# Optimization experiments

Measured on AMD Instinct MI355X. Metric: run time of the kernel, lower is better.

The kernel has to match this reference:

```python
import jax, jax.numpy as jnp
import numpy as np

N_NODES = 20000
N_EDGES = 320000
EMB = 128


def setup_inputs() -> dict:
    key = jax.random.key(0)
    ks = jax.random.split(key, 8)
    h = jax.random.normal(ks[0], (N_NODES, EMB), dtype=jnp.float32)
    W1 = jax.random.normal(ks[1], (2 * EMB, 4 * EMB), dtype=jnp.float32) / np.sqrt(2 * EMB)
    b1 = jnp.zeros((4 * EMB,), dtype=jnp.float32)
    W2 = jax.random.normal(ks[2], (4 * EMB, 1), dtype=jnp.float32) / np.sqrt(4 * EMB)
    b2 = jnp.zeros((1,), dtype=jnp.float32)
    # logistic-noise uniforms for RelaxedBernoulli rsample, kept away from {0,1}
    u = jax.random.uniform(ks[3], (N_EDGES,), dtype=jnp.float32, minval=1e-6, maxval=1.0 - 1e-6)
    row = jax.random.randint(ks[4], (N_EDGES,), 0, N_NODES, dtype=jnp.int32)
    col = jax.random.randint(ks[5], (N_EDGES,), 0, N_NODES, dtype=jnp.int32)
    edge_mask = -jnp.ones((N_EDGES,), dtype=jnp.int32)  # torch code initializes mask to -1
    return {"h": h, "W1": W1, "b1": b1, "W2": W2, "b2": b2,
            "u": u, "row": row, "col": col, "edge_mask": edge_mask, "hierarchy": 0}


def _segment_softmax(scores, seg, num_segments):
    m = jax.ops.segment_max(scores, seg, num_segments=num_segments)
    e = jnp.exp(scores - m[seg])
    s = jax.ops.segment_sum(e, seg, num_segments=num_segments)
    return e / s[seg]


TEMPERATURE = 1.0
RATIO = 0.5  # threshold for hard bernoulli


def reference(h, W1, b1, W2, b2, u, row, col, edge_mask, hierarchy):
    # edge gather + concat: [E, 2*EMB]
    edge_rep = jnp.concatenate([h[row], h[col]], axis=-1)
    # 2-layer MLP edge scorer -> [E]
    hid = jax.nn.relu(edge_rep @ W1 + b1)
    scores = (hid @ W2 + b2).reshape(-1)
    # segment softmax over edges grouped by source node (torch: softmax(edge_score, edge_index[0]))
    probs = _segment_softmax(scores, row, N_NODES)
    # RelaxedBernoulli(temperature, probs).rsample(): sigmoid((logits + logistic)/T)
    logits = jnp.log(probs) - jnp.log1p(-probs)
    logistic = jnp.log(u) - jnp.log1p(-u)
    y = jax.nn.sigmoid((logits + logistic) / TEMPERATURE)
    y_hard = (y > RATIO).astype(y.dtype)
    y_st = jax.lax.stop_gradient(y_hard - y) + y  # straight-through
    # edge_mask[y == 1] = hierarchy + 1
    new_mask = jnp.where(y_st == 1.0, jnp.int32(hierarchy + 1), edge_mask)
    c_idx = new_mask > 0
    s_idx = new_mask == -1
    causal_w = jnp.where(c_idx, scores, 0.0)
    spu_w = jnp.where(s_idx, -scores, 0.0)
    return scores, y_st, new_mask, causal_w, spu_w
```

## Files before the change

### kernel.cpp

```cpp
#include <hip/hip_runtime.h>
#include <math.h>

#define N_NODES 20000
#define N_EDGES 320000
#define EMB 128
#define HID 512
#define ROWS_PER_BLOCK 16
#define SC_CAP 2048
#define NCHUNK ((N_NODES + 1023) / 1024)

typedef float v2f __attribute__((ext_vector_type(2)));

#if defined(__has_builtin)
#if __has_builtin(__builtin_elementwise_fma)
#define V2FMA(a, b, c) __builtin_elementwise_fma((a), (b), (c))
#else
#define V2FMA(a, b, c) ((a) * (b) + (c))
#endif
#else
#define V2FMA(a, b, c) ((a) * (b) + (c))
#endif

__global__ void init_deg(int* __restrict__ deg, int* __restrict__ offs) {
    int i = blockIdx.x * 256 + threadIdx.x;
    if (i < N_NODES) deg[i] = 0;
    if (i == 0) offs[N_NODES] = N_EDGES;
}

#define TM 128
#define TN 128
#define BK 8
#define NTILES (EMB / BK)
#define GEMM_MT ((N_NODES + TM - 1) / TM)
#define GEMM_BLOCKS (8 * GEMM_MT)
#define HIST_BLOCKS ((N_EDGES + 255) / 256)

__global__ __launch_bounds__(256) void gemm_hist(
    const float* __restrict__ h, const float* __restrict__ W1,
    const float* __restrict__ b1, float* __restrict__ P, float* __restrict__ Q,
    const int* __restrict__ row, int* __restrict__ deg)
{
    const int bid = blockIdx.x;
    const int tid = threadIdx.x;

    if (bid >= GEMM_BLOCKS) {
        const int e = (bid - GEMM_BLOCKS) * 256 + tid;
        if (e < N_EDGES) atomicAdd(&deg[row[e]], 1);
        return;
    }

    __shared__ float As[2][BK][TM + 4];
    __shared__ float Bs[2][BK][TN];

    const int nt = bid & 7;
    const int mt = bid >> 3;
    const int m_base = mt * TM;

    const int a_m = tid >> 1;
    const int a_k = (tid & 1) << 2;
    const int  row_a = m_base + a_m;
    const bool a_ok  = row_a < N_NODES;
    const float* __restrict__ hrow = h + (size_t)row_a * EMB + a_k;

    const int b_k = tid >> 5;
    const int b_n = (tid & 31) << 2;
    const int w_row_off = (nt < 4) ? 0 : 128;
    const int w_col     = (nt & 3) * TN + b_n;
    const float* __restrict__ wrow = W1 + (size_t)(w_row_off + b_k) * HID + w_col;

    const int ty = tid >> 4, tx = tid & 15;
    const int cm = ty << 2, cn = tx << 2;

    v2f acc[8][4] = {};

    float4 pa, pb;
    pa = make_float4(0.f, 0.f, 0.f, 0.f);
    if (a_ok) pa = *(const float4*)(hrow);
    pb = *(const float4*)(wrow);
    As[0][a_k + 0][a_m] = pa.x;
    As[0][a_k + 1][a_m] = pa.y;
    As[0][a_k + 2][a_m] = pa.z;
    As[0][a_k + 3][a_m] = pa.w;
    *(float4*)&Bs[0][b_k][b_n] = pb;
    __syncthreads();

    for (int t = 0; t < NTILES; ++t) {
        const int cur = t & 1;
        if (t + 1 < NTILES) {
            const int k0 = (t + 1) * BK;
            pa = make_float4(0.f, 0.f, 0.f, 0.f);
            if (a_ok) pa = *(const float4*)(hrow + k0);
            pb = *(const float4*)(wrow + (size_t)k0 * HID);
        }

#pragma unroll
        for (int kk = 0; kk < BK; ++kk) {
            float a[8];
            *(float4*)&a[0] = *(const float4*)&As[cur][kk][cm];
            *(float4*)&a[4] = *(const float4*)&As[cur][kk][cm + 64];
            float4 b0 = *(const float4*)&Bs[cur][kk][cn];
            float4 b1v = *(const float4*)&Bs[cur][kk][cn + 64];
            v2f bp[4] = {(v2f){b0.x, b0.y}, (v2f){b0.z, b0.w},
                         (v2f){b1v.x, b1v.y}, (v2f){b1v.z, b1v.w}};
#pragma unroll
            for (int i = 0; i < 8; ++i) {
                v2f ai = (v2f){a[i], a[i]};
#pragma unroll
                for (int j = 0; j < 4; ++j)
                    acc[i][j] = V2FMA(ai, bp[j], acc[i][j]);
            }
        }

        if (t + 1 < NTILES) {
            const int nxt = 1 - cur;
            As[nxt][a_k + 0][a_m] = pa.x;
            As[nxt][a_k + 1][a_m] = pa.y;
            As[nxt][a_k + 2][a_m] = pa.z;
            As[nxt][a_k + 3][a_m] = pa.w;
            *(float4*)&Bs[nxt][b_k][b_n] = pb;
            __syncthreads();
        }
    }

    const bool  isP = (nt < 4);
    const int   col_base = (nt & 3) * TN;
    float* __restrict__ dstbase = isP ? P : Q;

    v2f bias[4] = {{0.f,0.f},{0.f,0.f},{0.f,0.f},{0.f,0.f}};
    if (isP) {
        float4 bv0 = *(const float4*)(b1 + col_base + cn);
        float4 bv1 = *(const float4*)(b1 + col_base + cn + 64);
        bias[0] = (v2f){bv0.x, bv0.y};
        bias[1] = (v2f){bv0.z, bv0.w};
        bias[2] = (v2f){bv1.x, bv1.y};
        bias[3] = (v2f){bv1.z, bv1.w};
    }

#pragma unroll
    for (int i = 0; i < 8; ++i) {
        const int r = m_base + cm + (i < 4 ? i : 64 + i - 4);
        if (r < N_NODES) {
            float* dst = dstbase + (size_t)r * HID + col_base;
            v2f c0 = acc[i][0] + bias[0], c1 = acc[i][1] + bias[1];
            v2f c2 = acc[i][2] + bias[2], c3 = acc[i][3] + bias[3];
            *(float4*)(dst + cn)      = make_float4(c0.x, c0.y, c1.x, c1.y);
            *(float4*)(dst + cn + 64) = make_float4(c2.x, c2.y, c3.x, c3.y);
        }
    }
}

__device__ __forceinline__ int wave_incl_scan(int v, int lane) {
#pragma unroll
    for (int off = 1; off < 64; off <<= 1) {
        int t = __shfl_up(v, off, 64);
        if (lane >= off) v += t;
    }
    return v;
}

__global__ __launch_bounds__(1024) void scan_part(const int* __restrict__ deg,
                                                  int* __restrict__ part,
                                                  int* __restrict__ totals) {
    __shared__ int wsum[16];
    const int tid = threadIdx.x, lane = tid & 63, w = tid >> 6;
    const int i = blockIdx.x * 1024 + tid;
    int v = (i < N_NODES) ? deg[i] : 0;
    int incl = wave_incl_scan(v, lane);
    if (lane == 63) wsum[w] = incl;
    __syncthreads();
    if (w == 0) {
        int x = (lane < 16) ? wsum[lane] : 0;
        int xs = wave_incl_scan(x, lane);
        if (lane < 16) wsum[lane] = xs - x;
        if (lane == 15) totals[blockIdx.x] = xs;
    }
    __syncthreads();
    if (i < N_NODES) part[i] = wsum[w] + incl - v;
}

__global__ __launch_bounds__(1024) void scan_apply(const int* __restrict__ part,
                                                   const int* __restrict__ totals,
                                                   int* __restrict__ cursor,
                                                   int* __restrict__ offs) {
    __shared__ int carry_s;
    const int tid = threadIdx.x;
    if (tid < 64) {
        int v = (tid < NCHUNK) ? totals[tid] : 0;
        int incl = wave_incl_scan(v, tid);
        if (tid == (int)blockIdx.x) carry_s = incl - v;
    }
    __syncthreads();
    const int i = blockIdx.x * 1024 + tid;
    if (i < N_NODES) {
        int o = part[i] + carry_s;
        cursor[i] = o;
        offs[i] = o;
    }
}

__global__ void scatter_edges(const int* __restrict__ row, const int* __restrict__ col,
                              int* __restrict__ cursor, int2* __restrict__ rc2) {
    int e = blockIdx.x * 256 + threadIdx.x;
    if (e >= N_EDGES) return;
    int r = row[e];
    int pos = atomicAdd(&cursor[r], 1);
    rc2[pos] = make_int2(e, (r << 16) | col[e]);
}

__global__ __launch_bounds__(256) void fused_edge(
    const float* __restrict__ P, const float* __restrict__ Q,
    const float* __restrict__ W2, const float* __restrict__ b2,
    const int2* __restrict__ rc2, const int* __restrict__ offs,
    const float* __restrict__ u, const int* __restrict__ edge_mask,
    const int* __restrict__ hierarchy,
    float* __restrict__ scores, float* __restrict__ out_y,
    float* __restrict__ out_mask, float* __restrict__ out_causal,
    float* __restrict__ out_spu)
{
    __shared__ float sc_lds[SC_CAP];

    const int r0 = blockIdx.x * ROWS_PER_BLOCK;
    const int r1 = (r0 + ROWS_PER_BLOCK < N_NODES) ? r0 + ROWS_PER_BLOCK : N_NODES;
    const int e0 = offs[r0];
    const int e1 = offs[r1];
    const int tid = threadIdx.x, lane = tid & 63, w = tid >> 6;
    const int j0 = lane << 2;

    const float4 w0 = *(const float4*)(W2 + j0);
    const float4 w1 = *(const float4*)(W2 + 256 + j0);
    const float bias2 = b2[0];

    for (int i0 = e0 + (w << 1); i0 < e1; i0 += 8) {
        const int  iA   = i0;
        const bool hasB = (i0 + 1) < e1;
        const int  iB   = hasB ? i0 + 1 : i0;

        const int2 eA = rc2[iA];
        const int2 eB = rc2[iB];
        const int rA = ((unsigned)eA.y) >> 16, cA = eA.y & 0xFFFF;
        const int rB = ((unsigned)eB.y) >> 16, cB = eB.y & 0xFFFF;
        const float* __restrict__ pA = P + (size_t)rA * HID;
        const float* __restrict__ qA = Q + (size_t)cA * HID;
        const float* __restrict__ pB = P + (size_t)rB * HID;
        const float* __restrict__ qB = Q + (size_t)cB * HID;

        float4 pA0 = *(const float4*)(pA + j0);
        float4 pA1 = *(const float4*)(pA + 256 + j0);
        float4 qA0 = *(const float4*)(qA + j0);
        float4 qA1 = *(const float4*)(qA + 256 + j0);
        float4 pB0 = *(const float4*)(pB + j0);
        float4 pB1 = *(const float4*)(pB + 256 + j0);
        float4 qB0 = *(const float4*)(qB + j0);
        float4 qB1 = *(const float4*)(qB + 256 + j0);

        float sA = 0.0f, sB = 0.0f;
        sA = fmaf(fmaxf(pA0.x + qA0.x, 0.0f), w0.x, sA);
        sA = fmaf(fmaxf(pA0.y + qA0.y, 0.0f), w0.y, sA);
        sA = fmaf(fmaxf(pA0.z + qA0.z, 0.0f), w0.z, sA);
        sA = fmaf(fmaxf(pA0.w + qA0.w, 0.0f), w0.w, sA);
        sA = fmaf(fmaxf(pA1.x + qA1.x, 0.0f), w1.x, sA);
        sA = fmaf(fmaxf(pA1.y + qA1.y, 0.0f), w1.y, sA);
        sA = fmaf(fmaxf(pA1.z + qA1.z, 0.0f), w1.z, sA);
        sA = fmaf(fmaxf(pA1.w + qA1.w, 0.0f), w1.w, sA);
        sB = fmaf(fmaxf(pB0.x + qB0.x, 0.0f), w0.x, sB);
        sB = fmaf(fmaxf(pB0.y + qB0.y, 0.0f), w0.y, sB);
        sB = fmaf(fmaxf(pB0.z + qB0.z, 0.0f), w0.z, sB);
        sB = fmaf(fmaxf(pB0.w + qB0.w, 0.0f), w0.w, sB);
        sB = fmaf(fmaxf(pB1.x + qB1.x, 0.0f), w1.x, sB);
        sB = fmaf(fmaxf(pB1.y + qB1.y, 0.0f), w1.y, sB);
        sB = fmaf(fmaxf(pB1.z + qB1.z, 0.0f), w1.z, sB);
        sB = fmaf(fmaxf(pB1.w + qB1.w, 0.0f), w1.w, sB);

#pragma unroll
        for (int off = 32; off > 0; off >>= 1) {
            sA += __shfl_down(sA, off, 64);
            sB += __shfl_down(sB, off, 64);
        }

        if (lane == 0) {
            float scA = sA + bias2;
            scores[eA.x] = scA;
            int liA = iA - e0;
            if (liA < SC_CAP) sc_lds[liA] = scA;
            if (hasB) {
                float scB = sB + bias2;
                scores[eB.x] = scB;
                int liB = iB - e0;
                if (liB < SC_CAP) sc_lds[liB] = scB;
            }
        }
    }
    __syncthreads();

    const int hv = hierarchy[0];
    for (int r = r0 + w; r < r1; r += 4) {
        const int es = offs[r], ee = offs[r + 1];
        const int d = ee - es;
        if (d == 0) continue;

        float m = -INFINITY;
        for (int j = lane; j < d; j += 64) {
            int li = es - e0 + j;
            float s = (li < SC_CAP) ? sc_lds[li] : scores[rc2[es + j].x];
            m = fmaxf(m, s);
        }
#pragma unroll
        for (int off = 32; off > 0; off >>= 1)
            m = fmaxf(m, __shfl_down(m, off, 64));
        m = __shfl(m, 0, 64);

        float ssum = 0.0f;
        for (int j = lane; j < d; j += 64) {
            int li = es - e0 + j;
            float s = (li < SC_CAP) ? sc_lds[li] : scores[rc2[es + j].x];
            ssum += expf(s - m);
        }
#pragma unroll
        for (int off = 32; off > 0; off >>= 1)
            ssum += __shfl_down(ssum, off, 64);
        ssum = __shfl(ssum, 0, 64);

        for (int j = lane; j < d; j += 64) {
            int li = es - e0 + j;
            float s = (li < SC_CAP) ? sc_lds[li] : scores[rc2[es + j].x];
            float p = expf(s - m) / ssum;
            float logits = logf(p) - log1pf(-p);
            int oe = rc2[es + j].x;
            float uu = u[oe];
            float L = logf(uu) - log1pf(-uu);
            float y = 1.0f / (1.0f + expf(-(logits + L)));
            bool hard = y > 0.5f;
            int mm = hard ? (hv + 1) : edge_mask[oe];
            out_y[oe]      = hard ? 1.0f : 0.0f;
            out_mask[oe]   = (float)mm;
            out_causal[oe] = (mm > 0)   ?  s : 0.0f;
            out_spu[oe]    = (mm == -1) ? -s : 0.0f;
        }
    }
}

extern "C" void kernel_launch(void* const* d_in, const int* in_sizes, int n_in,
                              void* d_out, int out_size, void* d_ws, size_t ws_size,
                              hipStream_t stream) {
    const float* h_ptr = (const float*)d_in[0];
    const float* W1    = (const float*)d_in[1];
    const float* b1    = (const float*)d_in[2];
    const float* W2    = (const float*)d_in[3];
    const float* b2    = (const float*)d_in[4];
    const float* u     = (const float*)d_in[5];
    const int*   row   = (const int*)d_in[6];
    const int*   col   = (const int*)d_in[7];
    const int*   emask = (const int*)d_in[8];
    const int*   hier  = (const int*)d_in[9];

    float* out        = (float*)d_out;
    float* scores     = out;
    float* out_y      = out + (size_t)N_EDGES;
    float* out_mask   = out + 2 * (size_t)N_EDGES;
    float* out_causal = out + 3 * (size_t)N_EDGES;
    float* out_spu    = out + 4 * (size_t)N_EDGES;

    float* P      = (float*)d_ws;
    float* Qm     = P + (size_t)N_NODES * HID;
    int2*  rc2    = (int2*)(Qm + (size_t)N_NODES * HID);
    int*   deg    = (int*)(rc2 + N_EDGES);
    int*   cursor = deg + N_NODES;
    int*   offs   = cursor + N_NODES;
    int*   part   = offs + N_NODES + 1;
    int*   totals = part + N_NODES;

    hipLaunchKernelGGL(init_deg, dim3((N_NODES + 255) / 256), dim3(256), 0, stream,
                       deg, offs);

    hipLaunchKernelGGL(gemm_hist, dim3(GEMM_BLOCKS + HIST_BLOCKS), dim3(256), 0, stream,
                       h_ptr, W1, b1, P, Qm, row, deg);

    hipLaunchKernelGGL(scan_part, dim3(NCHUNK), dim3(1024), 0, stream, deg, part, totals);
    hipLaunchKernelGGL(scan_apply, dim3(NCHUNK), dim3(1024), 0, stream,
                       part, totals, cursor, offs);
    hipLaunchKernelGGL(scatter_edges, dim3((N_EDGES + 255) / 256), dim3(256), 0, stream,
                       row, col, cursor, rc2);

    hipLaunchKernelGGL(fused_edge, dim3((N_NODES + ROWS_PER_BLOCK - 1) / ROWS_PER_BLOCK),
                       dim3(256), 0, stream,
                       P, Qm, W2, b2, rc2, offs, u, emask, hier,
                       scores, out_y, out_mask, out_causal, out_spu);
}
```

Baseline: 287.4 us.

## Process edges per source row with reused P row and coalesced unpermute pass

```diff
diff --git a/kernel.cpp b/kernel.cpp
--- a/kernel.cpp
+++ b/kernel.cpp
@@ -199,144 +199,165 @@
 }
 
 __global__ void scatter_edges(const int* __restrict__ row, const int* __restrict__ col,
-                              int* __restrict__ cursor, int2* __restrict__ rc2) {
+                              int* __restrict__ cursor,
+                              unsigned short* __restrict__ cols16,
+                              int* __restrict__ inv) {
     int e = blockIdx.x * 256 + threadIdx.x;
     if (e >= N_EDGES) return;
     int r = row[e];
     int pos = atomicAdd(&cursor[r], 1);
-    rc2[pos] = make_int2(e, (r << 16) | col[e]);
+    cols16[pos] = (unsigned short)col[e];
+    inv[e] = pos;
 }
 
 __global__ __launch_bounds__(256) void fused_edge(
     const float* __restrict__ P, const float* __restrict__ Q,
     const float* __restrict__ W2, const float* __restrict__ b2,
-    const int2* __restrict__ rc2, const int* __restrict__ offs,
+    const unsigned short* __restrict__ cols16, const int* __restrict__ offs,
+    float2* __restrict__ tmp)
+{
+    __shared__ float sc_lds[SC_CAP];
+
+    const int r0 = blockIdx.x * ROWS_PER_BLOCK;
+    const int r1 = (r0 + ROWS_PER_BLOCK < N_NODES) ? r0 + ROWS_PER_BLOCK : N_NODES;
+    const int e0 = offs[r0];
+    const int tid = threadIdx.x, lane = tid & 63, w = tid >> 6;
+    const int j0 = lane << 2;
+
+    const float4 w0 = *(const float4*)(W2 + j0);
+    const float4 w1 = *(const float4*)(W2 + 256 + j0);
+    const float bias2 = b2[0];
+
+    for (int r = r0 + w; r < r1; r += 4) {
+        const int es = offs[r], ee = offs[r + 1];
+        const int d = ee - es;
+        if (d == 0) continue;
+
+        const float* __restrict__ prow = P + (size_t)r * HID;
+        const float4 p0 = *(const float4*)(prow + j0);
+        const float4 p1 = *(const float4*)(prow + 256 + j0);
+
+        for (int base = 0; base < d; base += 64) {
+            const int nch = (d - base < 64) ? d - base : 64;
+            int mycol = 0;
+            if (lane < nch) mycol = (int)cols16[es + base + lane];
+
+#define QL(k, bb, d0, d1) { \
+                int c_ = __shfl(mycol, (bb) + (k), 64); \
+                const float* __restrict__ q_ = Q + (size_t)c_ * HID; \
+                d0 = *(const float4*)(q_ + j0); \
+                d1 = *(const float4*)(q_ + 256 + j0); }
+
+            float4 q00,q01,q10,q11,q20,q21,q30,q31;
+            QL(0,0,q00,q01); QL(1,0,q10,q11); QL(2,0,q20,q21); QL(3,0,q30,q31);
+
+            for (int b = 0; b < nch; b += 4) {
+                float4 n00,n01,n10,n11,n20,n21,n30,n31;
+                const bool more = (b + 4) < nch;
+                if (more) {
+                    QL(0,b+4,n00,n01); QL(1,b+4,n10,n11);
+                    QL(2,b+4,n20,n21); QL(3,b+4,n30,n31);
+                }
+
+                float s0, s1, s2, s3;
+#define DOT8(qa, qb, sd) { \
+                    float t_ = 0.0f; \
+                    t_ = fmaf(fmaxf(p0.x + qa.x, 0.0f), w0.x, t_); \
+                    t_ = fmaf(fmaxf(p0.y + qa.y, 0.0f), w0.y, t_); \
+                    t_ = fmaf(fmaxf(p0.z + qa.z, 0.0f), w0.z, t_); \
+                    t_ = fmaf(fmaxf(p0.w + qa.w, 0.0f), w0.w, t_); \
+                    t_ = fmaf(fmaxf(p1.x + qb.x, 0.0f), w1.x, t_); \
+                    t_ = fmaf(fmaxf(p1.y + qb.y, 0.0f), w1.y, t_); \
+                    t_ = fmaf(fmaxf(p1.z + qb.z, 0.0f), w1.z, t_); \
+                    t_ = fmaf(fmaxf(p1.w + qb.w, 0.0f), w1.w, t_); \
+                    sd = t_; }
+                DOT8(q00,q01,s0); DOT8(q10,q11,s1);
+                DOT8(q20,q21,s2); DOT8(q30,q31,s3);
+
+#pragma unroll
+                for (int off = 32; off > 0; off >>= 1) {
+                    s0 += __shfl_down(s0, off, 64);
+                    s1 += __shfl_down(s1, off, 64);
+                    s2 += __shfl_down(s2, off, 64);
+                    s3 += __shfl_down(s3, off, 64);
+                }
+
+                if (lane == 0) {
+                    const int nv = nch - b;
+                    const int libase = es - e0 + base + b;
+                    { float sc = s0 + bias2; int li = libase;
+                      if (li < SC_CAP) sc_lds[li] = sc; else tmp[e0 + li].x = sc; }
+                    if (nv > 1) { float sc = s1 + bias2; int li = libase + 1;
+                      if (li < SC_CAP) sc_lds[li] = sc; else tmp[e0 + li].x = sc; }
+                    if (nv > 2) { float sc = s2 + bias2; int li = libase + 2;
+                      if (li < SC_CAP) sc_lds[li] = sc; else tmp[e0 + li].x = sc; }
+                    if (nv > 3) { float sc = s3 + bias2; int li = libase + 3;
+                      if (li < SC_CAP) sc_lds[li] = sc; else tmp[e0 + li].x = sc; }
+                }
+
+                if (more) {
+                    q00=n00; q01=n01; q10=n10; q11=n11;
+                    q20=n20; q21=n21; q30=n30; q31=n31;
+                }
+            }
+#undef QL
+#undef DOT8
+        }
+
+        float m = -INFINITY;
+        for (int j = lane; j < d; j += 64) {
+            const int li = es - e0 + j;
+            float s = (li < SC_CAP) ? sc_lds[li] : tmp[es + j].x;
+            m = fmaxf(m, s);
+        }
+#pragma unroll
+        for (int off = 32; off > 0; off >>= 1)
+            m = fmaxf(m, __shfl_down(m, off, 64));
+        m = __shfl(m, 0, 64);
+
+        float ssum = 0.0f;
+        for (int j = lane; j < d; j += 64) {
+            const int li = es - e0 + j;
+            float s = (li < SC_CAP) ? sc_lds[li] : tmp[es + j].x;
+            ssum += expf(s - m);
+        }
+#pragma unroll
+        for (int off = 32; off > 0; off >>= 1)
+            ssum += __shfl_down(ssum, off, 64);
+        ssum = __shfl(ssum, 0, 64);
+
+        for (int j = lane; j < d; j += 64) {
+            const int li = es - e0 + j;
+            float s = (li < SC_CAP) ? sc_lds[li] : tmp[es + j].x;
+            float p = expf(s - m) / ssum;
+            float logits = logf(p) - log1pf(-p);
+            tmp[es + j] = make_float2(s, logits);
+        }
+    }
+}
+
+__global__ __launch_bounds__(256) void unperm(
+    const float2* __restrict__ tmp, const int* __restrict__ inv,
     const float* __restrict__ u, const int* __restrict__ edge_mask,
     const int* __restrict__ hierarchy,
     float* __restrict__ scores, float* __restrict__ out_y,
     float* __restrict__ out_mask, float* __restrict__ out_causal,
     float* __restrict__ out_spu)
 {
-    __shared__ float sc_lds[SC_CAP];
-
-    const int r0 = blockIdx.x * ROWS_PER_BLOCK;
-    const int r1 = (r0 + ROWS_PER_BLOCK < N_NODES) ? r0 + ROWS_PER_BLOCK : N_NODES;
-    const int e0 = offs[r0];
-    const int e1 = offs[r1];
-    const int tid = threadIdx.x, lane = tid & 63, w = tid >> 6;
-    const int j0 = lane << 2;
-
-    const float4 w0 = *(const float4*)(W2 + j0);
-    const float4 w1 = *(const float4*)(W2 + 256 + j0);
-    const float bias2 = b2[0];
-
-    for (int i0 = e0 + (w << 1); i0 < e1; i0 += 8) {
-        const int  iA   = i0;
-        const bool hasB = (i0 + 1) < e1;
-        const int  iB   = hasB ? i0 + 1 : i0;
-
-        const int2 eA = rc2[iA];
-        const int2 eB = rc2[iB];
-        const int rA = ((unsigned)eA.y) >> 16, cA = eA.y & 0xFFFF;
-        const int rB = ((unsigned)eB.y) >> 16, cB = eB.y & 0xFFFF;
-        const float* __restrict__ pA = P + (size_t)rA * HID;
-        const float* __restrict__ qA = Q + (size_t)cA * HID;
-        const float* __restrict__ pB = P + (size_t)rB * HID;
-        const float* __restrict__ qB = Q + (size_t)cB * HID;
-
-        float4 pA0 = *(const float4*)(pA + j0);
-        float4 pA1 = *(const float4*)(pA + 256 + j0);
-        float4 qA0 = *(const float4*)(qA + j0);
-        float4 qA1 = *(const float4*)(qA + 256 + j0);
-        float4 pB0 = *(const float4*)(pB + j0);
-        float4 pB1 = *(const float4*)(pB + 256 + j0);
-        float4 qB0 = *(const float4*)(qB + j0);
-        float4 qB1 = *(const float4*)(qB + 256 + j0);
-
-        float sA = 0.0f, sB = 0.0f;
-        sA = fmaf(fmaxf(pA0.x + qA0.x, 0.0f), w0.x, sA);
-        sA = fmaf(fmaxf(pA0.y + qA0.y, 0.0f), w0.y, sA);
-        sA = fmaf(fmaxf(pA0.z + qA0.z, 0.0f), w0.z, sA);
-        sA = fmaf(fmaxf(pA0.w + qA0.w, 0.0f), w0.w, sA);
-        sA = fmaf(fmaxf(pA1.x + qA1.x, 0.0f), w1.x, sA);
-        sA = fmaf(fmaxf(pA1.y + qA1.y, 0.0f), w1.y, sA);
-        sA = fmaf(fmaxf(pA1.z + qA1.z, 0.0f), w1.z, sA);
-        sA = fmaf(fmaxf(pA1.w + qA1.w, 0.0f), w1.w, sA);
-        sB = fmaf(fmaxf(pB0.x + qB0.x, 0.0f), w0.x, sB);
-        sB = fmaf(fmaxf(pB0.y + qB0.y, 0.0f), w0.y, sB);
-        sB = fmaf(fmaxf(pB0.z + qB0.z, 0.0f), w0.z, sB);
-        sB = fmaf(fmaxf(pB0.w + qB0.w, 0.0f), w0.w, sB);
-        sB = fmaf(fmaxf(pB1.x + qB1.x, 0.0f), w1.x, sB);
-        sB = fmaf(fmaxf(pB1.y + qB1.y, 0.0f), w1.y, sB);
-        sB = fmaf(fmaxf(pB1.z + qB1.z, 0.0f), w1.z, sB);
-        sB = fmaf(fmaxf(pB1.w + qB1.w, 0.0f), w1.w, sB);
-
-#pragma unroll
-        for (int off = 32; off > 0; off >>= 1) {
-            sA += __shfl_down(sA, off, 64);
-            sB += __shfl_down(sB, off, 64);
-        }
-
-        if (lane == 0) {
-            float scA = sA + bias2;
-            scores[eA.x] = scA;
-            int liA = iA - e0;
-            if (liA < SC_CAP) sc_lds[liA] = scA;
-            if (hasB) {
-                float scB = sB + bias2;
-                scores[eB.x] = scB;
-                int liB = iB - e0;
-                if (liB < SC_CAP) sc_lds[liB] = scB;
-            }
-        }
-    }
-    __syncthreads();
-
-    const int hv = hierarchy[0];
-    for (int r = r0 + w; r < r1; r += 4) {
-        const int es = offs[r], ee = offs[r + 1];
-        const int d = ee - es;
-        if (d == 0) continue;
-
-        float m = -INFINITY;
-        for (int j = lane; j < d; j += 64) {
-            int li = es - e0 + j;
-            float s = (li < SC_CAP) ? sc_lds[li] : scores[rc2[es + j].x];
-            m = fmaxf(m, s);
-        }
-#pragma unroll
-        for (int off = 32; off > 0; off >>= 1)
-            m = fmaxf(m, __shfl_down(m, off, 64));
-        m = __shfl(m, 0, 64);
-
-        float ssum = 0.0f;
-        for (int j = lane; j < d; j += 64) {
-            int li = es - e0 + j;
-            float s = (li < SC_CAP) ? sc_lds[li] : scores[rc2[es + j].x];
-            ssum += expf(s - m);
-        }
-#pragma unroll
-        for (int off = 32; off > 0; off >>= 1)
-            ssum += __shfl_down(ssum, off, 64);
-        ssum = __shfl(ssum, 0, 64);
-
-        for (int j = lane; j < d; j += 64) {
-            int li = es - e0 + j;
-            float s = (li < SC_CAP) ? sc_lds[li] : scores[rc2[es + j].x];
-            float p = expf(s - m) / ssum;
-            float logits = logf(p) - log1pf(-p);
-            int oe = rc2[es + j].x;
-            float uu = u[oe];
-            float L = logf(uu) - log1pf(-uu);
-            float y = 1.0f / (1.0f + expf(-(logits + L)));
-            bool hard = y > 0.5f;
-            int mm = hard ? (hv + 1) : edge_mask[oe];
-            out_y[oe]      = hard ? 1.0f : 0.0f;
-            out_mask[oe]   = (float)mm;
-            out_causal[oe] = (mm > 0)   ?  s : 0.0f;
-            out_spu[oe]    = (mm == -1) ? -s : 0.0f;
-        }
-    }
+    const int e = blockIdx.x * 256 + threadIdx.x;
+    if (e >= N_EDGES) return;
+    const float2 t = tmp[inv[e]];
+    const float s = t.x;
+    const float uu = u[e];
+    const float L = logf(uu) - log1pf(-uu);
+    const float y = 1.0f / (1.0f + expf(-(t.y + L)));
+    const bool hard = y > 0.5f;
+    const int mm = hard ? (hierarchy[0] + 1) : edge_mask[e];
+    scores[e]     = s;
+    out_y[e]      = hard ? 1.0f : 0.0f;
+    out_mask[e]   = (float)mm;
+    out_causal[e] = (mm > 0)   ?  s : 0.0f;
+    out_spu[e]    = (mm == -1) ? -s : 0.0f;
 }
 
 extern "C" void kernel_launch(void* const* d_in, const int* in_sizes, int n_in,
@@ -360,14 +381,16 @@
     float* out_causal = out + 3 * (size_t)N_EDGES;
     float* out_spu    = out + 4 * (size_t)N_EDGES;
 
-    float* P      = (float*)d_ws;
-    float* Qm     = P + (size_t)N_NODES * HID;
-    int2*  rc2    = (int2*)(Qm + (size_t)N_NODES * HID);
-    int*   deg    = (int*)(rc2 + N_EDGES);
-    int*   cursor = deg + N_NODES;
-    int*   offs   = cursor + N_NODES;
-    int*   part   = offs + N_NODES + 1;
-    int*   totals = part + N_NODES;
+    float*          P      = (float*)d_ws;
+    float*          Qm     = P + (size_t)N_NODES * HID;
+    float2*         tmp    = (float2*)(Qm + (size_t)N_NODES * HID);
+    unsigned short* cols16 = (unsigned short*)(tmp + N_EDGES);
+    int*            inv    = (int*)(cols16 + N_EDGES);
+    int*            deg    = inv + N_EDGES;
+    int*            cursor = deg + N_NODES;
+    int*            offs   = cursor + N_NODES;
+    int*            part   = offs + N_NODES + 1;
+    int*            totals = part + N_NODES;
 
     hipLaunchKernelGGL(init_deg, dim3((N_NODES + 255) / 256), dim3(256), 0, stream,
                        deg, offs);
@@ -379,10 +402,13 @@
     hipLaunchKernelGGL(scan_apply, dim3(NCHUNK), dim3(1024), 0, stream,
                        part, totals, cursor, offs);
     hipLaunchKernelGGL(scatter_edges, dim3((N_EDGES + 255) / 256), dim3(256), 0, stream,
-                       row, col, cursor, rc2);
+                       row, col, cursor, cols16, inv);
 
     hipLaunchKernelGGL(fused_edge, dim3((N_NODES + ROWS_PER_BLOCK - 1) / ROWS_PER_BLOCK),
                        dim3(256), 0, stream,
-                       P, Qm, W2, b2, rc2, offs, u, emask, hier,
+                       P, Qm, W2, b2, cols16, offs, tmp);
+
+    hipLaunchKernelGGL(unperm, dim3((N_EDGES + 255) / 256), dim3(256), 0, stream,
+                       tmp, inv, u, emask, hier,
                        scores, out_y, out_mask, out_causal, out_spu);
 }
```

Result: faster. 280.0 us (-2.6%).
